# Performance work log

Hardware: AMD Instinct MI355X
Metric: run time of the kernel (lower is better)

Reference implementation:

```python
import jax, jax.numpy as jnp
import numpy as np

N, H, R, E = 100000, 128, 30, 600000
EPS = 1e-5  # BatchNorm1d default eps


def _rgcn_layer(h, src, dst, etype, W, root, bias):
    """PyG RGCNConv: out = h @ root + bias + sum_r scatter_mean_r(h[src] @ W[r]).
    Mean is per (dst, relation) edge count."""
    n = h.shape[0]
    r_count = W.shape[0]
    seg = dst * r_count + etype                      # combined (dst, rel) segment id
    deg = jax.ops.segment_sum(jnp.ones_like(etype, dtype=h.dtype), seg,
                              num_segments=n * r_count)
    norm = 1.0 / jnp.maximum(deg[seg], 1.0)          # (E,) per-edge mean weight

    def body(out, inp):
        Wr, r = inp
        xr = h @ Wr                                  # (N,H) relation-transformed feats
        contrib = jnp.where((etype == r)[:, None], xr[src] * norm[:, None], 0.0)
        return out + jax.ops.segment_sum(contrib, dst, num_segments=n), None

    out0 = h @ root + bias
    out, _ = jax.lax.scan(body, out0, (W, jnp.arange(r_count)))
    return out


def _bn_relu(h, gamma, beta):
    # BatchNorm1d in training mode: biased batch statistics over the node dim
    mu = h.mean(axis=0)
    var = h.var(axis=0)
    return jax.nn.relu((h - mu) * jax.lax.rsqrt(var + EPS) * gamma + beta)


def setup_inputs() -> dict:
    key = jax.random.key(0)
    ks = jax.random.split(key, 16)
    s = 1.0 / np.sqrt(H)
    return {
        "x": jnp.arange(N, dtype=jnp.int32),
        "edge_index": jax.random.randint(ks[0], (2, E), 0, N, dtype=jnp.int32),
        "edge_type": jax.random.randint(ks[1], (E,), 0, R, dtype=jnp.int32),
        "emb": jax.random.normal(ks[2], (N, H), jnp.float32) * s,
        "W1": jax.random.normal(ks[3], (R, H, H), jnp.float32) * s,
        "root1": jax.random.normal(ks[4], (H, H), jnp.float32) * s,
        "b1": jnp.zeros((H,), jnp.float32),
        "g1": jnp.ones((H,), jnp.float32),
        "be1": jnp.zeros((H,), jnp.float32),
        "W2": jax.random.normal(ks[5], (R, H, H), jnp.float32) * s,
        "root2": jax.random.normal(ks[6], (H, H), jnp.float32) * s,
        "b2": jnp.zeros((H,), jnp.float32),
        "g2": jnp.ones((H,), jnp.float32),
        "be2": jnp.zeros((H,), jnp.float32),
    }


def reference(x, edge_index, edge_type, emb, W1, root1, b1, g1, be1,
              W2, root2, b2, g2, be2):
    src, dst = edge_index[0], edge_index[1]
    h = emb[x]                                        # (N,H) embedding lookup
    h = _bn_relu(_rgcn_layer(h, src, dst, edge_type, W1, root1, b1), g1, be1)
    h = _bn_relu(_rgcn_layer(h, src, dst, edge_type, W2, root2, b2), g2, be2)
    return h  # dropout is identity (deterministic reference)
```

## Files before the change

### kernel.cpp

```cpp
#include <hip/hip_runtime.h>
#include <hip/hip_bf16.h>

#define NN 100000
#define HH 128
#define RR 30
#define RR2 15
#define NE 600000
#define TILE 64
#define EPAD (NE + RR * TILE)
#define NCHMAX (EPAD / TILE)
#define NB_PS ((NN + 255) / 256)
#define NBLK_BN 784
#define RPB_BN 128
#define DBKT 512
#define BN_EPS 1e-5f

typedef __bf16 v8bf __attribute__((ext_vector_type(8)));
typedef float  v4f  __attribute__((ext_vector_type(4)));
typedef unsigned int v4u __attribute__((ext_vector_type(4)));

static __device__ __forceinline__ unsigned short f2b(float f) {
    unsigned int u = __float_as_uint(f);
    unsigned int r = (u + 0x7FFF + ((u >> 16) & 1)) >> 16;
    return (unsigned short)r;
}

static __device__ __forceinline__ unsigned int pk_bf16(float lo, float hi) {
    unsigned int r;
    asm("v_cvt_pk_bf16_f32 %0, %1, %2" : "=v"(r) : "v"(lo), "v"(hi));
    return r;
}

__global__ void k_hist(const int* __restrict__ dst, const int* __restrict__ et,
                       unsigned int* __restrict__ deg16, int* __restrict__ cnt) {
    __shared__ int lh[RR];
    int t = threadIdx.x;
    if (t < RR) lh[t] = 0;
    __syncthreads();
    int i = blockIdx.x * blockDim.x + t;
    if (i < NE) {
        int d = dst[i], r = et[i];
        atomicAdd(&deg16[(size_t)d * RR2 + (r >> 1)], 1u << ((r & 1) * 16));
        atomicAdd(&lh[r], 1);
    }
    __syncthreads();
    if (t < RR && lh[t]) atomicAdd(&cnt[t], lh[t]);
}

__global__ void k_degsum(const unsigned int* __restrict__ deg16,
                         int* __restrict__ cnt_d) {
    int d = blockIdx.x * blockDim.x + threadIdx.x;
    if (d >= NN) return;
    int s = 0;
#pragma unroll
    for (int r2 = 0; r2 < RR2; ++r2) {
        unsigned int v = deg16[(size_t)d * RR2 + r2];
        s += (int)(v & 0xffffu) + (int)(v >> 16);
    }
    cnt_d[d] = s;
}

__global__ void k_scan(const int* __restrict__ cnt, int* __restrict__ cursor,
                       int* __restrict__ totals,
                       int* __restrict__ src_s, int* __restrict__ dst_s,
                       float* __restrict__ norm_s, int* __restrict__ dpos_s,
                       int* __restrict__ chunk_rel, int need_dst) {
    __shared__ int off[RR + 1];
    if (threadIdx.x == 0) {
        int acc = 0;
        for (int r = 0; r < RR; ++r) {
            off[r] = acc;
            acc += (cnt[r] + TILE - 1) / TILE;
        }
        off[RR] = acc;
        totals[0] = acc * TILE;
    }
    __syncthreads();
    for (int r = 0; r < RR; ++r) {
        for (int c = off[r] + (int)threadIdx.x; c < off[r + 1]; c += blockDim.x)
            chunk_rel[c] = r;
        int begin = off[r] * TILE + cnt[r];
        int end   = off[r + 1] * TILE;
        for (int p = begin + (int)threadIdx.x; p < end; p += blockDim.x) {
            src_s[p] = 0; norm_s[p] = 0.f;
            dpos_s[p] = NE;
            if (need_dst) dst_s[p] = 0;
        }
    }
    if (threadIdx.x == 0)
        for (int r = 0; r < RR; ++r) cursor[r] = off[r] * TILE;
}

__global__ void k_psum1(const int* __restrict__ c, int* __restrict__ bsum) {
    __shared__ int sh[256];
    int i = blockIdx.x * 256 + threadIdx.x;
    sh[threadIdx.x] = (i < NN) ? c[i] : 0;
    __syncthreads();
    for (int s = 128; s > 0; s >>= 1) {
        if (threadIdx.x < s) sh[threadIdx.x] += sh[threadIdx.x + s];
        __syncthreads();
    }
    if (threadIdx.x == 0) bsum[blockIdx.x] = sh[0];
}

__global__ void k_psum2(int* __restrict__ bsum) {
    __shared__ int sh[512];
    int t = threadIdx.x;
    sh[t] = (t < NB_PS) ? bsum[t] : 0;
    __syncthreads();
    if (t == 0) {
        int acc = 0;
        for (int b = 0; b < NB_PS; ++b) { int v = sh[b]; sh[b] = acc; acc += v; }
    }
    __syncthreads();
    if (t < NB_PS) bsum[t] = sh[t];
}

__global__ void k_psum3(const int* __restrict__ c, const int* __restrict__ bscan,
                        int* __restrict__ off, int* __restrict__ cur) {
    __shared__ int sh[256];
    int t = threadIdx.x;
    int i = blockIdx.x * 256 + t;
    int v = (i < NN) ? c[i] : 0;
    sh[t] = v;
    __syncthreads();
    for (int s = 1; s < 256; s <<= 1) {
        int a = (t >= s) ? sh[t - s] : 0;
        __syncthreads();
        sh[t] += a;
        __syncthreads();
    }
    int excl = sh[t] - v + bscan[blockIdx.x];
    if (i < NN) { off[i] = excl; cur[i] = excl; }
    if (i == 0) off[NN] = NE;
}

__global__ void k_dhist(const int* __restrict__ cnt_d, int* __restrict__ dhist) {
    __shared__ int lh[DBKT];
    for (int i = threadIdx.x; i < DBKT; i += 256) lh[i] = 0;
    __syncthreads();
    int d = blockIdx.x * 256 + threadIdx.x;
    if (d < NN) {
        int b = cnt_d[d]; b = b < DBKT - 1 ? b : DBKT - 1;
        atomicAdd(&lh[b], 1);
    }
    __syncthreads();
    for (int i = threadIdx.x; i < DBKT; i += 256)
        if (lh[i]) atomicAdd(&dhist[i], lh[i]);
}

__global__ void k_dprefix(const int* __restrict__ dhist, int* __restrict__ dcur) {
    __shared__ int sh[DBKT];
    int t = threadIdx.x;
    int v = dhist[t];
    sh[t] = v;
    __syncthreads();
    for (int s = 1; s < DBKT; s <<= 1) {
        int a = (t >= s) ? sh[t - s] : 0;
        __syncthreads();
        sh[t] += a;
        __syncthreads();
    }
    dcur[t] = sh[t] - v;
}

__global__ void k_dscatter(const int* __restrict__ cnt_d, int* __restrict__ dcur,
                           int* __restrict__ perm) {
    __shared__ int lh[DBKT], lbase[DBKT];
    for (int i = threadIdx.x; i < DBKT; i += 256) lh[i] = 0;
    __syncthreads();
    int d = blockIdx.x * 256 + threadIdx.x;
    int b = 0, lrank = 0;
    bool valid = (d < NN);
    if (valid) {
        b = cnt_d[d]; b = b < DBKT - 1 ? b : DBKT - 1;
        lrank = atomicAdd(&lh[b], 1);
    }
    __syncthreads();
    for (int i = threadIdx.x; i < DBKT; i += 256)
        if (lh[i]) lbase[i] = atomicAdd(&dcur[i], lh[i]);
    __syncthreads();
    if (valid) perm[lbase[b] + lrank] = d;
}

__global__ void k_scatter(const int* __restrict__ src, const int* __restrict__ dst,
                          const int* __restrict__ et,
                          const unsigned int* __restrict__ deg16,
                          int* __restrict__ cursor, int* __restrict__ cursor_dst,
                          int* __restrict__ src_s, int* __restrict__ dst_s,
                          float* __restrict__ norm_s, int* __restrict__ dpos_s,
                          int need_dst) {
    __shared__ int lh[RR];
    __shared__ int lbase[RR];
    int t = threadIdx.x;
    if (t < RR) lh[t] = 0;
    __syncthreads();
    int i = blockIdx.x * blockDim.x + t;
    int r = 0, d = 0, lrank = 0;
    bool valid = (i < NE);
    if (valid) {
        r = et[i]; d = dst[i];
        lrank = atomicAdd(&lh[r], 1);
    }
    __syncthreads();
    if (t < RR && lh[t]) lbase[t] = atomicAdd(&cursor[t], lh[t]);
    __syncthreads();
    if (valid) {
        int pos = lbase[r] + lrank;
        src_s[pos] = src[i];
        if (need_dst) dst_s[pos] = d;
        int dg = (int)((deg16[(size_t)d * RR2 + (r >> 1)] >> ((r & 1) * 16)) & 0xffffu);
        norm_s[pos] = 1.0f / (float)(dg > 1 ? dg : 1);
        dpos_s[pos] = atomicAdd(&cursor_dst[d], 1);
    }
}

__global__ void k_convW(const float* __restrict__ W, unsigned short* __restrict__ Wt,
                        int total) {
    int idx = blockIdx.x * blockDim.x + threadIdx.x;
    if (idx >= total) return;
    int m = idx / (HH * HH);
    int rem = idx % (HH * HH);
    int k = rem / HH, c = rem % HH;
    Wt[m * HH * HH + c * HH + k] = f2b(W[idx]);
}

__global__ void k_embed(const int* __restrict__ x, const float* __restrict__ emb,
                        unsigned int* __restrict__ hb2) {
    int idx = blockIdx.x * blockDim.x + threadIdx.x;
    if (idx >= NN * HH / 2) return;
    int i = idx >> 6;
    int j2 = (idx & 63) * 2;
    const float* p = emb + (size_t)x[i] * HH + j2;
    hb2[idx] = pk_bf16(p[0], p[1]);
}

__global__ __launch_bounds__(256) void k_rootagg(const unsigned short* __restrict__ hb,
                                                 const unsigned short* __restrict__ rootT,
                                                 const float* __restrict__ bias,
                                                 const int* __restrict__ off,
                                                 const int* __restrict__ perm,
                                                 const unsigned short* __restrict__ xe,
                                                 float* __restrict__ tmp) {
    __shared__ __align__(16) unsigned short Ws[64][HH + 8];
    int t = threadIdx.x;
    int base = blockIdx.x * TILE;

    int w = t >> 6, lane = t & 63;
    int lr16 = lane & 15, kg = lane >> 4;
    int slot = w * 16 + lr16;
    int pidx = base + slot;
    bool valid = (pidx < NN);
    int drow = valid ? perm[pidx] : 0;

    v8bf xf[4];
    const unsigned short* hrow = hb + (size_t)drow * HH + kg * 8;
#pragma unroll
    for (int kk = 0; kk < 4; ++kk)
        xf[kk] = *reinterpret_cast<const v8bf*>(hrow + kk * 32);

    v4f acc[8];
#pragma unroll
    for (int n = 0; n < 8; ++n) acc[n] = (v4f){0.f, 0.f, 0.f, 0.f};

    for (int i = 0; i < 4; ++i) {
        int idx = t + 256 * i;
        int row = idx >> 4, g = idx & 15;
        *reinterpret_cast<uint4*>(&Ws[row][g * 8]) =
            *reinterpret_cast<const uint4*>(rootT + row * HH + g * 8);
    }
    __syncthreads();
#pragma unroll
    for (int n = 0; n < 4; ++n)
#pragma unroll
        for (int kk = 0; kk < 4; ++kk) {
            v8bf wf = *reinterpret_cast<const v8bf*>(&Ws[n * 16 + lr16][kk * 32 + kg * 8]);
            acc[n] = __builtin_amdgcn_mfma_f32_16x16x32_bf16(wf, xf[kk], acc[n], 0, 0, 0);
        }
    __syncthreads();
    for (int i = 0; i < 4; ++i) {
        int idx = t + 256 * i;
        int row = idx >> 4, g = idx & 15;
        *reinterpret_cast<uint4*>(&Ws[row][g * 8]) =
            *reinterpret_cast<const uint4*>(rootT + (64 + row) * HH + g * 8);
    }
    __syncthreads();
#pragma unroll
    for (int n = 4; n < 8; ++n)
#pragma unroll
        for (int kk = 0; kk < 4; ++kk) {
            v8bf wf = *reinterpret_cast<const v8bf*>(&Ws[(n - 4) * 16 + lr16][kk * 32 + kg * 8]);
            acc[n] = __builtin_amdgcn_mfma_f32_16x16x32_bf16(wf, xf[kk], acc[n], 0, 0, 0);
        }

    int s = valid ? off[drow] : 0;
    int e = valid ? off[drow + 1] : 0;
    int p = s;
    for (; p + 1 < e; p += 2) {
        const unsigned short* xr0 = xe + (size_t)p * HH + kg * 4;
        const unsigned short* xr1 = xr0 + HH;
        uint2 u0[8], u1[8];
#pragma unroll
        for (int n = 0; n < 8; ++n) {
            u0[n] = *reinterpret_cast<const uint2*>(xr0 + n * 16);
            u1[n] = *reinterpret_cast<const uint2*>(xr1 + n * 16);
        }
#pragma unroll
        for (int n = 0; n < 8; ++n) {
            acc[n][0] += __uint_as_float(u0[n].x << 16) + __uint_as_float(u1[n].x << 16);
            acc[n][1] += __uint_as_float(u0[n].x & 0xffff0000u) + __uint_as_float(u1[n].x & 0xffff0000u);
            acc[n][2] += __uint_as_float(u0[n].y << 16) + __uint_as_float(u1[n].y << 16);
            acc[n][3] += __uint_as_float(u0[n].y & 0xffff0000u) + __uint_as_float(u1[n].y & 0xffff0000u);
        }
    }
    if (p < e) {
        const unsigned short* xr = xe + (size_t)p * HH + kg * 4;
#pragma unroll
        for (int n = 0; n < 8; ++n) {
            uint2 u = *reinterpret_cast<const uint2*>(xr + n * 16);
            acc[n][0] += __uint_as_float(u.x << 16);
            acc[n][1] += __uint_as_float(u.x & 0xffff0000u);
            acc[n][2] += __uint_as_float(u.y << 16);
            acc[n][3] += __uint_as_float(u.y & 0xffff0000u);
        }
    }

    if (valid) {
        float* orow = tmp + (size_t)drow * HH + kg * 4;
#pragma unroll
        for (int n = 0; n < 8; ++n) {
            v4f b = *reinterpret_cast<const v4f*>(bias + n * 16 + kg * 4);
            *reinterpret_cast<v4f*>(orow + n * 16) = acc[n] + b;
        }
    }
}

__global__ __launch_bounds__(256) void k_rootgemm(const unsigned short* __restrict__ hb,
                                                  const unsigned short* __restrict__ rootT,
                                                  const float* __restrict__ bias,
                                                  float* __restrict__ tmp) {
    __shared__ __align__(16) unsigned short Xs[TILE][HH + 8];
    __shared__ __align__(16) unsigned short Ws[HH][HH + 8];
    int base = blockIdx.x * TILE;
    int t = threadIdx.x;

    {
        int l = t >> 2, lr = t & 3;
        int row = base + l;
        for (int i = 0; i < 4; ++i) {
            int g = lr + 4 * i;
            uint4 v = {0u, 0u, 0u, 0u};
            if (row < NN) v = *reinterpret_cast<const uint4*>(hb + (size_t)row * HH + g * 8);
            *reinterpret_cast<uint4*>(&Xs[l][g * 8]) = v;
        }
    }
    for (int i = 0; i < 8; ++i) {
        int idx = t + 256 * i;
        int row = idx >> 4, g = idx & 15;
        *reinterpret_cast<uint4*>(&Ws[row][g * 8]) =
            *reinterpret_cast<const uint4*>(rootT + row * HH + g * 8);
    }
    __syncthreads();

    int w = t >> 6, lane = t & 63;
    int lr16 = lane & 15, kg = lane >> 4;
    v4f acc[8];
    for (int n = 0; n < 8; ++n) acc[n] = (v4f){0.f, 0.f, 0.f, 0.f};
#pragma unroll
    for (int kk = 0; kk < 4; ++kk) {
        int k0 = kk * 32 + kg * 8;
        v8bf a = *reinterpret_cast<const v8bf*>(&Xs[w * 16 + lr16][k0]);
#pragma unroll
        for (int n = 0; n < 8; ++n) {
            v8bf b = *reinterpret_cast<const v8bf*>(&Ws[n * 16 + lr16][k0]);
            acc[n] = __builtin_amdgcn_mfma_f32_16x16x32_bf16(a, b, acc[n], 0, 0, 0);
        }
    }
#pragma unroll
    for (int n = 0; n < 8; ++n)
        for (int j = 0; j < 4; ++j) {
            int row = base + w * 16 + kg * 4 + j;
            int col = n * 16 + lr16;
            if (row < NN) tmp[(size_t)row * HH + col] = acc[n][j] + bias[col];
        }
}

__global__ __launch_bounds__(256) void k_edgegemm_x(const unsigned short* __restrict__ hb,
                                                    const unsigned short* __restrict__ Wt,
                                                    const int* __restrict__ src_s,
                                                    const int* __restrict__ chunk_rel,
                                                    const float* __restrict__ norm_s,
                                                    const int* __restrict__ dpos_s,
                                                    const int* __restrict__ totals,
                                                    unsigned short* __restrict__ xe) {
    int ebase = blockIdx.x * TILE;
    if (ebase >= totals[0]) return;
    __shared__ __align__(16) unsigned short S[HH * (HH + 8)];
    int t = threadIdx.x;
    int rel = chunk_rel[blockIdx.x];

    const unsigned short* Wr = Wt + (size_t)rel * HH * HH;
    for (int i = 0; i < 8; ++i) {
        int idx = t + 256 * i;
        int row = idx >> 4, g = idx & 15;
        *reinterpret_cast<uint4*>(&S[row * (HH + 8) + g * 8]) =
            *reinterpret_cast<const uint4*>(Wr + row * HH + g * 8);
    }

    int w = t >> 6, lane = t & 63;
    int lr16 = lane & 15, kg = lane >> 4;
    int slot = w * 16 + lr16;
    int srow = src_s[ebase + slot];
    float nrm = norm_s[ebase + slot];

    v8bf xf[4];
    const unsigned short* hrow = hb + (size_t)srow * HH + kg * 8;
#pragma unroll
    for (int kk = 0; kk < 4; ++kk)
        xf[kk] = *reinterpret_cast<const v8bf*>(hrow + kk * 32);

    __syncthreads();

    v4f acc[8];
#pragma unroll
    for (int n = 0; n < 8; ++n) acc[n] = (v4f){0.f, 0.f, 0.f, 0.f};
#pragma unroll
    for (int n = 0; n < 8; ++n)
#pragma unroll
        for (int kk = 0; kk < 4; ++kk) {
            v8bf wf = *reinterpret_cast<const v8bf*>(
                &S[(n * 16 + lr16) * (HH + 8) + kk * 32 + kg * 8]);
            acc[n] = __builtin_amdgcn_mfma_f32_16x16x32_bf16(wf, xf[kk], acc[n], 0, 0, 0);
        }

    __syncthreads();

    int c = slot & 7;
#pragma unroll
    for (int n = 0; n < 8; ++n) {
        unsigned int w0 = pk_bf16(acc[n][0] * nrm, acc[n][1] * nrm);
        unsigned int w1 = pk_bf16(acc[n][2] * nrm, acc[n][3] * nrm);
        unsigned long long p = (unsigned long long)w0 | ((unsigned long long)w1 << 32);
        int a = n * 4 + kg;
        int sw = (((a >> 1) ^ c) << 1) | (a & 1);
        *reinterpret_cast<unsigned long long*>(&S[slot * HH + sw * 4]) = p;
    }
    __syncthreads();
    {
        int l = t >> 2, lr = t & 3;
        size_t drow = (size_t)dpos_s[ebase + l];
        int cs = l & 7;
        unsigned short* orow = xe + drow * HH;
#pragma unroll
        for (int i = 0; i < 4; ++i) {
            int j = lr + 4 * i;
            v4u v = *reinterpret_cast<const v4u*>(&S[l * HH + (j ^ cs) * 8]);
            *reinterpret_cast<v4u*>(orow + j * 8) = v;
        }
    }
}

__global__ __launch_bounds__(256) void k_edgegemm_at(const unsigned short* __restrict__ hb,
                                                     const unsigned short* __restrict__ Wt,
                                                     const int* __restrict__ src_s,
                                                     const int* __restrict__ dst_s,
                                                     const int* __restrict__ chunk_rel,
                                                     const float* __restrict__ norm_s,
                                                     const int* __restrict__ totals,
                                                     float* __restrict__ tmp) {
    int ebase = blockIdx.x * TILE;
    if (ebase >= totals[0]) return;
    __shared__ __align__(16) unsigned short Xs[TILE][HH + 8];
    __shared__ __align__(16) unsigned short Ws[HH][HH + 8];
    __shared__ int   src_l[TILE];
    __shared__ int   dst_l[TILE];
    __shared__ float nrm_l[TILE];
    int t = threadIdx.x;
    if (t < TILE) {
        src_l[t] = src_s[ebase + t];
        dst_l[t] = dst_s[ebase + t];
        nrm_l[t] = norm_s[ebase + t];
    }
    int rel = chunk_rel[blockIdx.x];
    __syncthreads();
    {
        int l = t >> 2, lr = t & 3;
        int srow = src_l[l];
        for (int i = 0; i < 4; ++i) {
            int g = lr + 4 * i;
            *reinterpret_cast<uint4*>(&Xs[l][g * 8]) =
                *reinterpret_cast<const uint4*>(hb + (size_t)srow * HH + g * 8);
        }
    }
    const unsigned short* Wr = Wt + (size_t)rel * HH * HH;
    for (int i = 0; i < 8; ++i) {
        int idx = t + 256 * i;
        int row = idx >> 4, g = idx & 15;
        *reinterpret_cast<uint4*>(&Ws[row][g * 8]) =
            *reinterpret_cast<const uint4*>(Wr + row * HH + g * 8);
    }
    __syncthreads();
    int w = t >> 6, lane = t & 63;
    int lr16 = lane & 15, kg = lane >> 4;
    v4f acc[8];
    for (int n = 0; n < 8; ++n) acc[n] = (v4f){0.f, 0.f, 0.f, 0.f};
#pragma unroll
    for (int kk = 0; kk < 4; ++kk) {
        int k0 = kk * 32 + kg * 8;
        v8bf a = *reinterpret_cast<const v8bf*>(&Xs[w * 16 + lr16][k0]);
#pragma unroll
        for (int n = 0; n < 8; ++n) {
            v8bf b = *reinterpret_cast<const v8bf*>(&Ws[n * 16 + lr16][k0]);
            acc[n] = __builtin_amdgcn_mfma_f32_16x16x32_bf16(a, b, acc[n], 0, 0, 0);
        }
    }
#pragma unroll
    for (int n = 0; n < 8; ++n)
        for (int j = 0; j < 4; ++j) {
            int slot = w * 16 + kg * 4 + j;
            int col  = n * 16 + lr16;
            atomicAdd(&tmp[(size_t)dst_l[slot] * HH + col], acc[n][j] * nrm_l[slot]);
        }
}

__global__ __launch_bounds__(256) void k_bnsum1(const float* __restrict__ tmp,
                                                float* __restrict__ psum,
                                                float* __restrict__ psq) {
    int t = threadIdx.x;
    int rg = t >> 5, lane = t & 31;
    int base = blockIdx.x * RPB_BN;
    v4f s = {0.f, 0.f, 0.f, 0.f}, q = {0.f, 0.f, 0.f, 0.f};
#pragma unroll 4
    for (int i = 0; i < RPB_BN / 8; ++i) {
        int row = base + rg + 8 * i;
        if (row < NN) {
            v4f v = *reinterpret_cast<const v4f*>(tmp + (size_t)row * HH + lane * 4);
            s += v; q += v * v;
        }
    }
    __shared__ v4f shs[8][32], shq[8][32];
    shs[rg][lane] = s; shq[rg][lane] = q;
    __syncthreads();
    if (rg == 0) {
        v4f ts = shs[0][lane], tq = shq[0][lane];
#pragma unroll
        for (int k = 1; k < 8; ++k) { ts += shs[k][lane]; tq += shq[k][lane]; }
        int b = blockIdx.x;
#pragma unroll
        for (int j = 0; j < 4; ++j) {
            psum[(size_t)(lane * 4 + j) * NBLK_BN + b] = ts[j];
            psq [(size_t)(lane * 4 + j) * NBLK_BN + b] = tq[j];
        }
    }
}

__global__ void k_bnsum2(const float* __restrict__ psum, const float* __restrict__ psq,
                         const float* __restrict__ g, const float* __restrict__ be,
                         float* __restrict__ sc_g, float* __restrict__ shf_g) {
    __shared__ float ssum[HH], ssq[HH];
    int t = threadIdx.x;
    int col = t & 127;
    const float* row = ((t < 128) ? psum : psq) + (size_t)col * NBLK_BN;
    v4f a = {0.f, 0.f, 0.f, 0.f};
    for (int i = 0; i < NBLK_BN / 4; ++i)
        a += *reinterpret_cast<const v4f*>(row + i * 4);
    float acc = a[0] + a[1] + a[2] + a[3];
    if (t < 128) ssum[col] = acc; else ssq[col] = acc;
    __syncthreads();
    if (t < 128) {
        float inv_n = 1.0f / (float)NN;
        float mean = ssum[col] * inv_n;
        float var = ssq[col] * inv_n - mean * mean;
        float sc = g[col] * rsqrtf(var + BN_EPS);
        sc_g[col] = sc;
        shf_g[col] = be[col] - mean * sc;
    }
}

__global__ void k_bnapply(const float* __restrict__ tmp, const float* __restrict__ sc_g,
                          const float* __restrict__ shf_g,
                          unsigned short* __restrict__ hout,
                          float* __restrict__ fout, int write_bf16) {
    int idx = blockIdx.x * blockDim.x + threadIdx.x;
    if (idx >= NN * HH / 4) return;
    int c4 = (idx & 31) * 4;
    v4f v  = *reinterpret_cast<const v4f*>(tmp + (size_t)idx * 4);
    v4f sc = *reinterpret_cast<const v4f*>(sc_g + c4);
    v4f sh = *reinterpret_cast<const v4f*>(shf_g + c4);
    v4f r;
#pragma unroll
    for (int j = 0; j < 4; ++j) r[j] = fmaxf(v[j] * sc[j] + sh[j], 0.f);
    if (write_bf16) {
        uint2 u;
        u.x = pk_bf16(r[0], r[1]);
        u.y = pk_bf16(r[2], r[3]);
        *reinterpret_cast<uint2*>(hout + (size_t)idx * 4) = u;
    } else {
        *reinterpret_cast<v4f*>(fout + (size_t)idx * 4) = r;
    }
}

constexpr size_t OFF_DEG  = 0;
constexpr size_t OFF_HB   = OFF_DEG + (size_t)NN * RR2 * 4;
constexpr size_t OFF_TMP  = OFF_HB + (size_t)NN * HH * 2;
constexpr size_t OFF_W1T  = OFF_TMP + (size_t)NN * HH * 4;
constexpr size_t OFF_W2T  = OFF_W1T + (size_t)RR * HH * HH * 2;
constexpr size_t OFF_R1T  = OFF_W2T + (size_t)RR * HH * HH * 2;
constexpr size_t OFF_R2T  = OFF_R1T + (size_t)HH * HH * 2;
constexpr size_t OFF_SRCS = OFF_R2T + (size_t)HH * HH * 2;
constexpr size_t OFF_DSTS = OFF_SRCS + (size_t)EPAD * 4;
constexpr size_t OFF_NRMS = OFF_DSTS + (size_t)EPAD * 4;
constexpr size_t OFF_DPOS = OFF_NRMS + (size_t)EPAD * 4;
constexpr size_t OFF_CREL = OFF_DPOS + (size_t)EPAD * 4;
constexpr size_t OFF_CNTD = OFF_CREL + ((size_t)NCHMAX * 4 + 255 & ~(size_t)255);
constexpr size_t OFF_OFFD = OFF_CNTD + ((size_t)(NN + 1) * 4 + 255 & ~(size_t)255);
constexpr size_t OFF_CURD = OFF_OFFD + ((size_t)(NN + 1) * 4 + 255 & ~(size_t)255);
constexpr size_t OFF_PERM = OFF_CURD + ((size_t)NN * 4 + 255 & ~(size_t)255);
constexpr size_t OFF_DH   = OFF_PERM + ((size_t)NN * 4 + 255 & ~(size_t)255);
constexpr size_t OFF_DC   = OFF_DH + DBKT * 4;
constexpr size_t OFF_BSUM = OFF_DC + DBKT * 4;
constexpr size_t OFF_CTRL = OFF_BSUM + ((size_t)NB_PS * 4 + 255 & ~(size_t)255);
constexpr size_t OFF_SC   = OFF_CTRL + 512;
constexpr size_t OFF_SHF  = OFF_SC + 512;
constexpr size_t OFF_PSUM = OFF_SHF + 512;
constexpr size_t OFF_PSQ  = OFF_PSUM + (size_t)HH * NBLK_BN * 4;
constexpr size_t OFF_XE   = (OFF_PSQ + (size_t)HH * NBLK_BN * 4 + 255) & ~(size_t)255;
constexpr size_t WS_MIN   = OFF_XE;
constexpr size_t WS_FULL  = OFF_XE + (size_t)EPAD * HH * 2;

extern "C" void kernel_launch(void* const* d_in, const int* in_sizes, int n_in,
                              void* d_out, int out_size, void* d_ws, size_t ws_size,
                              hipStream_t stream) {
    const int*   x     = (const int*)d_in[0];
    const int*   eidx  = (const int*)d_in[1];
    const int*   et    = (const int*)d_in[2];
    const float* emb   = (const float*)d_in[3];
    const float* W1    = (const float*)d_in[4];
    const float* root1 = (const float*)d_in[5];
    const float* b1    = (const float*)d_in[6];
    const float* g1    = (const float*)d_in[7];
    const float* be1   = (const float*)d_in[8];
    const float* W2    = (const float*)d_in[9];
    const float* root2 = (const float*)d_in[10];
    const float* b2    = (const float*)d_in[11];
    const float* g2    = (const float*)d_in[12];
    const float* be2   = (const float*)d_in[13];
    float* out = (float*)d_out;

    if (ws_size < WS_MIN) return;
    const bool full = (ws_size >= WS_FULL);
    const int need_dst = full ? 0 : 1;

    char* ws = (char*)d_ws;
    unsigned int* deg16 = (unsigned int*)(ws + OFF_DEG);
    unsigned short* hb = (unsigned short*)(ws + OFF_HB);
    float* tmp    = (float*)(ws + OFF_TMP);
    unsigned short* W1t = (unsigned short*)(ws + OFF_W1T);
    unsigned short* W2t = (unsigned short*)(ws + OFF_W2T);
    unsigned short* r1t = (unsigned short*)(ws + OFF_R1T);
    unsigned short* r2t = (unsigned short*)(ws + OFF_R2T);
    int*   src_s  = (int*)(ws + OFF_SRCS);
    int*   dst_s  = (int*)(ws + OFF_DSTS);
    float* norm_s = (float*)(ws + OFF_NRMS);
    int*   dpos_s = (int*)(ws + OFF_DPOS);
    int*   crel   = (int*)(ws + OFF_CREL);
    int*   cnt_d  = (int*)(ws + OFF_CNTD);
    int*   off_d  = (int*)(ws + OFF_OFFD);
    int*   cur_d  = (int*)(ws + OFF_CURD);
    int*   perm   = (int*)(ws + OFF_PERM);
    int*   dhist  = (int*)(ws + OFF_DH);
    int*   dcur   = (int*)(ws + OFF_DC);
    int*   bsum   = (int*)(ws + OFF_BSUM);
    int*   cnt    = (int*)(ws + OFF_CTRL);
    int*   cursor = cnt + 32;
    int*   totals = cnt + 64;
    float* sc_g   = (float*)(ws + OFF_SC);
    float* shf_g  = (float*)(ws + OFF_SHF);
    float* psum   = (float*)(ws + OFF_PSUM);
    float* psq    = (float*)(ws + OFF_PSQ);
    unsigned short* xe = (unsigned short*)(ws + OFF_XE);

    const int* srcp = eidx;
    const int* dstp = eidx + NE;

    hipMemsetAsync(deg16, 0, (size_t)NN * RR2 * 4, stream);
    hipMemsetAsync(cnt, 0, 512, stream);
    hipMemsetAsync(dhist, 0, DBKT * 4, stream);

    k_hist<<<(NE + 255) / 256, 256, 0, stream>>>(dstp, et, deg16, cnt);
    k_degsum<<<(NN + 255) / 256, 256, 0, stream>>>(deg16, cnt_d);
    k_scan<<<1, 256, 0, stream>>>(cnt, cursor, totals, src_s, dst_s, norm_s,
                                  dpos_s, crel, need_dst);
    k_psum1<<<NB_PS, 256, 0, stream>>>(cnt_d, bsum);
    k_psum2<<<1, 512, 0, stream>>>(bsum);
    k_psum3<<<NB_PS, 256, 0, stream>>>(cnt_d, bsum, off_d, cur_d);
    k_dhist<<<(NN + 255) / 256, 256, 0, stream>>>(cnt_d, dhist);
    k_dprefix<<<1, DBKT, 0, stream>>>(dhist, dcur);
    k_dscatter<<<(NN + 255) / 256, 256, 0, stream>>>(cnt_d, dcur, perm);
    k_scatter<<<(NE + 255) / 256, 256, 0, stream>>>(srcp, dstp, et, deg16, cursor, cur_d,
                                                    src_s, dst_s, norm_s, dpos_s,
                                                    need_dst);
    k_convW<<<(RR * HH * HH + 255) / 256, 256, 0, stream>>>(W1, W1t, RR * HH * HH);
    k_convW<<<(RR * HH * HH + 255) / 256, 256, 0, stream>>>(W2, W2t, RR * HH * HH);
    k_convW<<<(HH * HH + 255) / 256, 256, 0, stream>>>(root1, r1t, HH * HH);
    k_convW<<<(HH * HH + 255) / 256, 256, 0, stream>>>(root2, r2t, HH * HH);
    k_embed<<<(NN * HH / 2 + 255) / 256, 256, 0, stream>>>(x, emb, (unsigned int*)hb);

    const unsigned short* Wts[2] = {W1t, W2t};
    const unsigned short* rts[2] = {r1t, r2t};
    const float* biases[2] = {b1, b2};
    const float* gs[2]     = {g1, g2};
    const float* bes[2]    = {be1, be2};

    for (int layer = 0; layer < 2; ++layer) {
        if (full) {
            k_edgegemm_x<<<EPAD / TILE, 256, 0, stream>>>(hb, Wts[layer], src_s, crel,
                                                          norm_s, dpos_s, totals, xe);
            k_rootagg<<<(NN + TILE - 1) / TILE, 256, 0, stream>>>(hb, rts[layer],
                                                                  biases[layer], off_d,
                                                                  perm, xe, tmp);
        } else {
            k_rootgemm<<<(NN + TILE - 1) / TILE, 256, 0, stream>>>(hb, rts[layer],
                                                                   biases[layer], tmp);
            k_edgegemm_at<<<EPAD / TILE, 256, 0, stream>>>(hb, Wts[layer], src_s, dst_s,
                                                           crel, norm_s, totals, tmp);
        }
        k_bnsum1<<<NBLK_BN, 256, 0, stream>>>(tmp, psum, psq);
        k_bnsum2<<<1, 256, 0, stream>>>(psum, psq, gs[layer], bes[layer], sc_g, shf_g);
        k_bnapply<<<(NN * HH / 4 + 255) / 256, 256, 0, stream>>>(tmp, sc_g, shf_g,
                                                                 hb, out, layer == 0);
    }
}
```

Baseline: 506.1 us.

## Lay out per-destination edge segments in degree-sorted permutation order

Computes the destination CSR offsets over the degree-sorted node permutation instead of node id order. The edges of consecutive rows processed by k_rootagg then sit next to each other in the xe buffer, and the offset reads become coalesced. This is meant to improve memory locality in the aggregation loop. It adds two small gather/scatter kernels to the preprocessing stage.

```diff
diff --git a/kernel.cpp b/kernel.cpp
--- a/kernel.cpp
+++ b/kernel.cpp
@@ -183,6 +183,18 @@
     if (valid) perm[lbase[b] + lrank] = d;
 }
 
+__global__ void k_permcnt(const int* __restrict__ cnt_d, const int* __restrict__ perm,
+                          int* __restrict__ cnt_p) {
+    int i = blockIdx.x * blockDim.x + threadIdx.x;
+    if (i < NN) cnt_p[i] = cnt_d[perm[i]];
+}
+
+__global__ void k_permcur(const int* __restrict__ off2, const int* __restrict__ perm,
+                          int* __restrict__ cur_d) {
+    int i = blockIdx.x * blockDim.x + threadIdx.x;
+    if (i < NN) cur_d[perm[i]] = off2[i];
+}
+
 __global__ void k_scatter(const int* __restrict__ src, const int* __restrict__ dst,
                           const int* __restrict__ et,
                           const unsigned int* __restrict__ deg16,
@@ -238,7 +250,7 @@
 __global__ __launch_bounds__(256) void k_rootagg(const unsigned short* __restrict__ hb,
                                                  const unsigned short* __restrict__ rootT,
                                                  const float* __restrict__ bias,
-                                                 const int* __restrict__ off,
+                                                 const int* __restrict__ off2,
                                                  const int* __restrict__ perm,
                                                  const unsigned short* __restrict__ xe,
                                                  float* __restrict__ tmp) {
@@ -293,8 +305,8 @@
             acc[n] = __builtin_amdgcn_mfma_f32_16x16x32_bf16(wf, xf[kk], acc[n], 0, 0, 0);
         }
 
-    int s = valid ? off[drow] : 0;
-    int e = valid ? off[drow + 1] : 0;
+    int s = valid ? off2[pidx] : 0;
+    int e = valid ? off2[pidx + 1] : 0;
     int p = s;
     for (; p + 1 < e; p += 2) {
         const unsigned short* xr0 = xe + (size_t)p * HH + kg * 4;
@@ -613,8 +625,10 @@
 constexpr size_t OFF_DPOS = OFF_NRMS + (size_t)EPAD * 4;
 constexpr size_t OFF_CREL = OFF_DPOS + (size_t)EPAD * 4;
 constexpr size_t OFF_CNTD = OFF_CREL + ((size_t)NCHMAX * 4 + 255 & ~(size_t)255);
-constexpr size_t OFF_OFFD = OFF_CNTD + ((size_t)(NN + 1) * 4 + 255 & ~(size_t)255);
-constexpr size_t OFF_CURD = OFF_OFFD + ((size_t)(NN + 1) * 4 + 255 & ~(size_t)255);
+constexpr size_t OFF_CNTP = OFF_CNTD + ((size_t)(NN + 1) * 4 + 255 & ~(size_t)255);
+constexpr size_t OFF_OFFD = OFF_CNTP + ((size_t)(NN + 1) * 4 + 255 & ~(size_t)255);
+constexpr size_t OFF_CUR2 = OFF_OFFD + ((size_t)(NN + 1) * 4 + 255 & ~(size_t)255);
+constexpr size_t OFF_CURD = OFF_CUR2 + ((size_t)NN * 4 + 255 & ~(size_t)255);
 constexpr size_t OFF_PERM = OFF_CURD + ((size_t)NN * 4 + 255 & ~(size_t)255);
 constexpr size_t OFF_DH   = OFF_PERM + ((size_t)NN * 4 + 255 & ~(size_t)255);
 constexpr size_t OFF_DC   = OFF_DH + DBKT * 4;
@@ -665,7 +679,9 @@
     int*   dpos_s = (int*)(ws + OFF_DPOS);
     int*   crel   = (int*)(ws + OFF_CREL);
     int*   cnt_d  = (int*)(ws + OFF_CNTD);
-    int*   off_d  = (int*)(ws + OFF_OFFD);
+    int*   cnt_p  = (int*)(ws + OFF_CNTP);
+    int*   off2   = (int*)(ws + OFF_OFFD);
+    int*   cur2   = (int*)(ws + OFF_CUR2);
     int*   cur_d  = (int*)(ws + OFF_CURD);
     int*   perm   = (int*)(ws + OFF_PERM);
     int*   dhist  = (int*)(ws + OFF_DH);
@@ -691,12 +707,14 @@
     k_degsum<<<(NN + 255) / 256, 256, 0, stream>>>(deg16, cnt_d);
     k_scan<<<1, 256, 0, stream>>>(cnt, cursor, totals, src_s, dst_s, norm_s,
                                   dpos_s, crel, need_dst);
-    k_psum1<<<NB_PS, 256, 0, stream>>>(cnt_d, bsum);
-    k_psum2<<<1, 512, 0, stream>>>(bsum);
-    k_psum3<<<NB_PS, 256, 0, stream>>>(cnt_d, bsum, off_d, cur_d);
     k_dhist<<<(NN + 255) / 256, 256, 0, stream>>>(cnt_d, dhist);
     k_dprefix<<<1, DBKT, 0, stream>>>(dhist, dcur);
     k_dscatter<<<(NN + 255) / 256, 256, 0, stream>>>(cnt_d, dcur, perm);
+    k_permcnt<<<(NN + 255) / 256, 256, 0, stream>>>(cnt_d, perm, cnt_p);
+    k_psum1<<<NB_PS, 256, 0, stream>>>(cnt_p, bsum);
+    k_psum2<<<1, 512, 0, stream>>>(bsum);
+    k_psum3<<<NB_PS, 256, 0, stream>>>(cnt_p, bsum, off2, cur2);
+    k_permcur<<<(NN + 255) / 256, 256, 0, stream>>>(off2, perm, cur_d);
     k_scatter<<<(NE + 255) / 256, 256, 0, stream>>>(srcp, dstp, et, deg16, cursor, cur_d,
                                                     src_s, dst_s, norm_s, dpos_s,
                                                     need_dst);
@@ -717,7 +735,7 @@
             k_edgegemm_x<<<EPAD / TILE, 256, 0, stream>>>(hb, Wts[layer], src_s, crel,
                                                           norm_s, dpos_s, totals, xe);
             k_rootagg<<<(NN + TILE - 1) / TILE, 256, 0, stream>>>(hb, rts[layer],
-                                                                  biases[layer], off_d,
+                                                                  biases[layer], off2,
                                                                   perm, xe, tmp);
         } else {
             k_rootgemm<<<(NN + TILE - 1) / TILE, 256, 0, stream>>>(hb, rts[layer],
```

After: 506.0 us. No clear change (-0.0%).
